# Performance work log

Hardware: AMD Instinct MI355X
Metric: run time of the kernel (lower is better)

Reference implementation:

```python
import jax, jax.numpy as jnp
import numpy as np

D_MODEL = 1024
N_HEAD = 16
N_KV_HEAD = 4
D_K = D_MODEL // N_HEAD          # 64
N_REP = N_HEAD // N_KV_HEAD      # 4
B, S = 2, 2048


def setup_inputs() -> dict:
    key = jax.random.key(0)
    ks = jax.random.split(key, 7)
    scale = 1.0 / np.sqrt(D_MODEL)
    return {
        "q": jax.random.normal(ks[0], (B, S, D_MODEL), jnp.float32),
        "k": jax.random.normal(ks[1], (B, S, D_MODEL), jnp.float32),
        "v": jax.random.normal(ks[2], (B, S, D_MODEL), jnp.float32),
        # weights stored [in, out] (nn.Linear applies x @ W.T; we fold the transpose)
        "W_q": jax.random.normal(ks[3], (D_MODEL, N_HEAD * D_K), jnp.float32) * scale,
        "W_k": jax.random.normal(ks[4], (D_MODEL, N_KV_HEAD * D_K), jnp.float32) * scale,
        "W_v": jax.random.normal(ks[5], (D_MODEL, N_KV_HEAD * D_K), jnp.float32) * scale,
        "W_o": jax.random.normal(ks[6], (D_MODEL, D_MODEL), jnp.float32) * scale,
    }


def reference(q, k, v, W_q, W_k, W_v, W_o):
    batch, seq_q, _ = q.shape
    seq_k = k.shape[1]
    # projections -> [b, h, s, d]
    Q = (q @ W_q).reshape(batch, seq_q, N_HEAD, D_K).transpose(0, 2, 1, 3)
    K = (k @ W_k).reshape(batch, seq_k, N_KV_HEAD, D_K).transpose(0, 2, 1, 3)
    V = (v @ W_v).reshape(batch, seq_k, N_KV_HEAD, D_K).transpose(0, 2, 1, 3)
    # repeat each KV head n_rep times consecutively (matches expand+reshape)
    K = jnp.repeat(K, N_REP, axis=1)  # [b, n_head, seq_k, d_k]
    V = jnp.repeat(V, N_REP, axis=1)
    scores = jnp.einsum('bhqd,bhkd->bhqk', Q, K) / np.sqrt(D_K).astype(jnp.float32)
    attn = jax.nn.softmax(scores, axis=-1)
    out = jnp.einsum('bhqk,bhkd->bhqd', attn, V)  # [b, h, seq_q, d_k]
    out = out.transpose(0, 2, 1, 3).reshape(batch, seq_q, D_MODEL)
    return out @ W_o
```

## Files before the change

kernel.cpp:

```cpp
#include <hip/hip_runtime.h>
#include <hip/hip_bf16.h>
#include <stdint.h>

#define DEVINL __device__ __forceinline__

typedef unsigned short u16;
typedef __bf16 bf16x8 __attribute__((ext_vector_type(8)));
typedef float f32x4 __attribute__((ext_vector_type(4)));
typedef float f32x16 __attribute__((ext_vector_type(16)));
typedef unsigned short u16x8 __attribute__((ext_vector_type(8)));
typedef unsigned int u32x4 __attribute__((ext_vector_type(4)));

constexpr int BATCH = 2, SEQ = 2048, DM = 1024, NH = 16, NKVH = 4, DK = 64;
#define QSCALE 0.18033688f

DEVINL u16 f2bf(float f) {
    unsigned u = __builtin_bit_cast(unsigned, f);
    u += 0x7fffu + ((u >> 16) & 1u);
    return (u16)(u >> 16);
}

DEVINL unsigned pkbf(float a, float b) {
    unsigned r;
    asm("v_cvt_pk_bf16_f32 %0, %1, %2" : "=v"(r) : "v"(a), "v"(b));
    return r;
}
DEVINL void swap32(unsigned& a, unsigned& b) {
    asm("v_permlane32_swap_b32 %0, %1" : "+v"(a), "+v"(b));
}
DEVINL float fexp2(float x) {
    float r;
    asm("v_exp_f32 %0, %1" : "=v"(r) : "v"(x));
    return r;
}

DEVINL void gload16(const void* g, void* l) {
    __builtin_amdgcn_global_load_lds(
        (const __attribute__((address_space(1))) unsigned int*)g,
        (__attribute__((address_space(3))) unsigned int*)l, 16, 0, 0);
}

DEVINL bf16x8 ldfrag(const u16* p) { return *reinterpret_cast<const bf16x8*>(p); }

__global__ __launch_bounds__(256) void prep_kernel(
    const float* __restrict__ Wq, const float* __restrict__ Wk,
    const float* __restrict__ Wv, const float* __restrict__ Wo,
    u16* __restrict__ Wqt, u16* __restrict__ Wkt,
    u16* __restrict__ Wvt, u16* __restrict__ Wot) {
    __shared__ float tile[32][33];
    int bid = blockIdx.x;
    int z = bid >> 10, rem = bid & 1023;
    const float* W;
    u16* Wt;
    int N;
    switch (z) {
        case 0: W = Wq; Wt = Wqt; N = 1024; break;
        case 1: W = Wk; Wt = Wkt; N = 256; break;
        case 2: W = Wv; Wt = Wvt; N = 256; break;
        default: W = Wo; Wt = Wot; N = 1024; break;
    }
    int n0 = (rem & 31) * 32;
    if (n0 >= N) return;
    int k0 = (rem >> 5) * 32;
    int tx = threadIdx.x & 31, ty = threadIdx.x >> 5;
#pragma unroll
    for (int r = 0; r < 4; ++r)
        tile[ty + 8 * r][tx] = W[(size_t)(k0 + ty + 8 * r) * N + n0 + tx];
    __syncthreads();
#pragma unroll
    for (int r = 0; r < 4; ++r)
        Wt[(size_t)(n0 + ty + 8 * r) * 1024 + k0 + tx] = f2bf(tile[tx][ty + 8 * r]);
}

#define GEMM_CORE64(Apt, Bpt)                                                 \
    __shared__ __align__(16) u16 Al[2][128 * 64];                             \
    __shared__ __align__(16) u16 Bl[2][64 * 64];                              \
    const int tid = threadIdx.x;                                              \
    const int lane = tid & 63;                                                \
    const int w = tid >> 6;                                                   \
    const u16* Ab = (Apt) + (size_t)m0 * 1024;                                \
    const u16* Bb = (Bpt) + (size_t)n0 * 1024;                                \
    f32x4 acc[2][4] = {};                                                     \
    auto stage = [&](int buf, int kt) {                                       \
        _Pragma("unroll") for (int rnd = 0; rnd < 4; ++rnd) {                 \
            int L = tid * 16 + rnd * 4096;                                    \
            int row = L >> 7;                                                 \
            int cb = (L & 127) ^ ((row & 7) << 4);                            \
            gload16(Ab + (size_t)row * 1024 + kt * 64 + (cb >> 1),            \
                    &Al[buf][L >> 1]);                                        \
        }                                                                     \
        _Pragma("unroll") for (int rnd = 0; rnd < 2; ++rnd) {                 \
            int L = tid * 16 + rnd * 4096;                                    \
            int row = L >> 7;                                                 \
            int cb = (L & 127) ^ ((row & 7) << 4);                            \
            gload16(Bb + (size_t)row * 1024 + kt * 64 + (cb >> 1),            \
                    &Bl[buf][L >> 1]);                                        \
        }                                                                     \
    };                                                                        \
    stage(0, 0);                                                              \
    __syncthreads();                                                          \
    int buf = 0;                                                              \
    for (int kt = 0; kt < 16; ++kt) {                                         \
        if (kt + 1 < 16) stage(buf ^ 1, kt + 1);                              \
        bf16x8 af[2][2], bfr[2][4];                                           \
        _Pragma("unroll") for (int kk = 0; kk < 2; ++kk)                      \
            _Pragma("unroll") for (int mi = 0; mi < 2; ++mi) {                \
                int row = w * 32 + mi * 16 + (lane & 15);                     \
                int cb = (kk * 64 + (lane >> 4) * 16) ^ ((row & 7) << 4);     \
                af[kk][mi] = ldfrag(&Al[buf][row * 64 + (cb >> 1)]);          \
            }                                                                 \
        _Pragma("unroll") for (int kk = 0; kk < 2; ++kk)                      \
            _Pragma("unroll") for (int ni = 0; ni < 4; ++ni) {                \
                int row = ni * 16 + (lane & 15);                              \
                int cb = (kk * 64 + (lane >> 4) * 16) ^ ((row & 7) << 4);     \
                bfr[kk][ni] = ldfrag(&Bl[buf][row * 64 + (cb >> 1)]);         \
            }                                                                 \
        _Pragma("unroll") for (int kk = 0; kk < 2; ++kk)                      \
            _Pragma("unroll") for (int mi = 0; mi < 2; ++mi)                  \
                _Pragma("unroll") for (int ni = 0; ni < 4; ++ni)              \
                    acc[mi][ni] = __builtin_amdgcn_mfma_f32_16x16x32_bf16(    \
                        af[kk][mi], bfr[kk][ni], acc[mi][ni], 0, 0, 0);       \
        __syncthreads();                                                      \
        buf ^= 1;                                                             \
    }

__global__ __launch_bounds__(256) void proj_kernel(
    const float* __restrict__ q32, const float* __restrict__ k32, const float* __restrict__ v32,
    const u16* __restrict__ Wqt, const u16* __restrict__ Wkt, const u16* __restrict__ Wvt,
    u16* __restrict__ Qp, u16* __restrict__ Kf, u16* __restrict__ Vf) {
    int bid = blockIdx.x;
    int tile = (bid & 7) * 96 + (bid >> 3);
    const float* A32;
    const u16* Bt;
    int m0, n0, z;
    if (tile < 512) {
        z = 0; A32 = q32; Bt = Wqt; m0 = (tile >> 4) * 128; n0 = (tile & 15) * 64;
    } else if (tile < 640) {
        int t = tile - 512;
        z = 1; A32 = k32; Bt = Wkt; m0 = (t >> 2) * 128; n0 = (t & 3) * 64;
    } else {
        int t = tile - 640;
        z = 2; A32 = v32; Bt = Wvt; m0 = (t >> 2) * 128; n0 = (t & 3) * 64;
    }

    __shared__ __align__(16) u16 Al[2][128 * 64];
    __shared__ __align__(16) u16 Bl[2][64 * 64];
    const int tid = threadIdx.x;
    const int lane = tid & 63;
    const int w = tid >> 6;
    const float* Ab32 = A32 + (size_t)m0 * 1024;
    const u16* Bb = Bt + (size_t)n0 * 1024;
    f32x4 acc[2][4] = {};

    int adst[4];
    const float* asrc[4];
#pragma unroll
    for (int rnd = 0; rnd < 4; ++rnd) {
        int L = tid * 16 + rnd * 4096;
        int row = L >> 7, colb = L & 127;
        adst[rnd] = (row * 128 + (colb ^ ((row & 7) << 4)));
        asrc[rnd] = Ab32 + (size_t)row * 1024 + (colb >> 1);
    }
    const int LB = tid * 16;
    const int brow0 = LB >> 7;
    const int bcb0 = (LB & 127) ^ ((brow0 & 7) << 4);
    const int LB1 = LB + 4096;
    const int brow1 = LB1 >> 7;
    const int bcb1 = (LB1 & 127) ^ ((brow1 & 7) << 4);

    auto stageB = [&](int buf, int kt) {
        gload16(Bb + (size_t)brow0 * 1024 + kt * 64 + (bcb0 >> 1), &Bl[buf][LB >> 1]);
        gload16(Bb + (size_t)brow1 * 1024 + kt * 64 + (bcb1 >> 1), &Bl[buf][LB1 >> 1]);
    };
    auto packwr = [&](int buf, const float4& a, const float4& b, int dst) {
        u32x4 pk;
        pk[0] = pkbf(a.x, a.y); pk[1] = pkbf(a.z, a.w);
        pk[2] = pkbf(b.x, b.y); pk[3] = pkbf(b.z, b.w);
        *(u32x4*)((char*)&Al[buf][0] + dst) = pk;
    };

    {
        stageB(0, 0);
#pragma unroll
        for (int rnd = 0; rnd < 4; ++rnd) {
            float4 a = *(const float4*)asrc[rnd];
            float4 b = *(const float4*)(asrc[rnd] + 4);
            packwr(0, a, b, adst[rnd]);
        }
    }
    __syncthreads();

    int buf = 0;
    for (int kt = 0; kt < 16; ++kt) {
        float4 a4[4], b4[4];
        if (kt + 1 < 16) {
            stageB(buf ^ 1, kt + 1);
#pragma unroll
            for (int rnd = 0; rnd < 4; ++rnd) {
                const float* s = asrc[rnd] + (kt + 1) * 64;
                a4[rnd] = *(const float4*)s;
                b4[rnd] = *(const float4*)(s + 4);
            }
        }
        bf16x8 af[2][2], bfr[2][4];
#pragma unroll
        for (int kk = 0; kk < 2; ++kk)
#pragma unroll
            for (int mi = 0; mi < 2; ++mi) {
                int row = w * 32 + mi * 16 + (lane & 15);
                int cb = (kk * 64 + (lane >> 4) * 16) ^ ((row & 7) << 4);
                af[kk][mi] = ldfrag(&Al[buf][row * 64 + (cb >> 1)]);
            }
#pragma unroll
        for (int kk = 0; kk < 2; ++kk)
#pragma unroll
            for (int ni = 0; ni < 4; ++ni) {
                int row = ni * 16 + (lane & 15);
                int cb = (kk * 64 + (lane >> 4) * 16) ^ ((row & 7) << 4);
                bfr[kk][ni] = ldfrag(&Bl[buf][row * 64 + (cb >> 1)]);
            }
#pragma unroll
        for (int kk = 0; kk < 2; ++kk)
#pragma unroll
            for (int mi = 0; mi < 2; ++mi)
#pragma unroll
                for (int ni = 0; ni < 4; ++ni)
                    acc[mi][ni] = __builtin_amdgcn_mfma_f32_16x16x32_bf16(
                        af[kk][mi], bfr[kk][ni], acc[mi][ni], 0, 0, 0);
        if (kt + 1 < 16) {
#pragma unroll
            for (int rnd = 0; rnd < 4; ++rnd)
                packwr(buf ^ 1, a4[rnd], b4[rnd], adst[rnd]);
        }
        __syncthreads();
        buf ^= 1;
    }

#pragma unroll
    for (int mi = 0; mi < 2; ++mi)
#pragma unroll
        for (int ni = 0; ni < 4; ++ni)
#pragma unroll
            for (int r = 0; r < 4; ++r) {
                int row = m0 + w * 32 + mi * 16 + (lane >> 4) * 4 + r;
                int col = n0 + ni * 16 + (lane & 15);
                float v = acc[mi][ni][r];
                int bb = row >> 11, s = row & 2047;
                int hh = col >> 6, dd = col & 63;
                if (z == 0) {
                    Qp[((((size_t)bb * NH + hh) * 2048 + s) << 6) + dd] = f2bf(v * QSCALE);
                } else if (z == 1) {
                    size_t base = (size_t)(bb * NKVH + hh) * 131072;
                    int s32 = s >> 5, q31s = s & 31;
                    int c = dd >> 4, hib = (dd >> 3) & 1, j = dd & 7;
                    Kf[base + (size_t)((s32 * 4 + c) * 64 + hib * 32 + q31s) * 8 + j] = f2bf(v);
                } else {
                    size_t base = (size_t)(bb * NKVH + hh) * 131072;
                    int kt = s >> 6, i = (s >> 4) & 3, hib = (s >> 3) & 1, j = s & 7;
                    int dt = dd >> 5, q31v = dd & 31;
                    Vf[base + (size_t)((((kt * 2 + dt) * 4 + i) * 64) + hib * 32 + q31v) * 8 + j] = f2bf(v);
                }
            }
}

__global__ __launch_bounds__(256) void oproj_kernel(const u16* __restrict__ Oa,
                                                    const u16* __restrict__ Wot,
                                                    float* __restrict__ out) {
    int bid = blockIdx.x;
    int tile = (bid & 7) * 64 + (bid >> 3);
    const int m0 = (tile >> 4) * 128, n0 = (tile & 15) * 64;

    GEMM_CORE64(Oa, Wot)

#pragma unroll
    for (int mi = 0; mi < 2; ++mi)
#pragma unroll
        for (int ni = 0; ni < 4; ++ni)
#pragma unroll
            for (int r = 0; r < 4; ++r) {
                int row = m0 + w * 32 + mi * 16 + (lane >> 4) * 4 + r;
                int col = n0 + ni * 16 + (lane & 15);
                out[(size_t)row * 1024 + col] = acc[mi][ni][r];
            }
}

__global__ __launch_bounds__(256) void attn_kernel(const u16* __restrict__ Qp,
                                                   const u16* __restrict__ Kf,
                                                   const u16* __restrict__ Vf,
                                                   u16* __restrict__ Oa) {
    const int tid = threadIdx.x;
    const int lane = tid & 63, w = tid >> 6;
    const int hi = lane >> 5, q31 = lane & 31;
    const int qt = blockIdx.x, h = blockIdx.y, b = blockIdx.z;
    const int kvh = h >> 2;
    const int qrow = qt * 128 + w * 32 + q31;

    const u16* Qb = Qp + ((size_t)((b * NH + h) * SEQ) + qrow) * 64 + hi * 8;
    bf16x8 qf0 = ldfrag(Qb), qf1 = ldfrag(Qb + 16);
    bf16x8 qf2 = ldfrag(Qb + 32), qf3 = ldfrag(Qb + 48);

    const u16* Kb = Kf + (size_t)(b * NKVH + kvh) * 131072 + lane * 8;
    const u16* Vb = Vf + (size_t)(b * NKVH + kvh) * 131072 + lane * 8;

    bf16x8 k0[8], k1[8], vf[8];
#pragma unroll
    for (int r = 0; r < 8; ++r) k0[r] = ldfrag(Kb + (size_t)r * 512);
#pragma unroll
    for (int r = 0; r < 8; ++r) k1[r] = ldfrag(Kb + (size_t)(8 + r) * 512);
#pragma unroll
    for (int r = 0; r < 8; ++r) vf[r] = ldfrag(Vb + (size_t)r * 512);

    u16x8 ov;
#pragma unroll
    for (int j = 0; j < 8; ++j) ov[j] = 0x3F80;
    const bf16x8 ones = __builtin_bit_cast(bf16x8, ov);

    f32x16 od0 = {}, od1 = {}, lacc = {};
    f32x16 sA0 = {}, sA1 = {}, sB0 = {}, sB1 = {};

    sA0 = __builtin_amdgcn_mfma_f32_32x32x16_bf16(k0[0], qf0, sA0, 0, 0, 0);
    sA1 = __builtin_amdgcn_mfma_f32_32x32x16_bf16(k0[4], qf0, sA1, 0, 0, 0);
    sA0 = __builtin_amdgcn_mfma_f32_32x32x16_bf16(k0[1], qf1, sA0, 0, 0, 0);
    sA1 = __builtin_amdgcn_mfma_f32_32x32x16_bf16(k0[5], qf1, sA1, 0, 0, 0);
    sA0 = __builtin_amdgcn_mfma_f32_32x32x16_bf16(k0[2], qf2, sA0, 0, 0, 0);
    sA1 = __builtin_amdgcn_mfma_f32_32x32x16_bf16(k0[6], qf2, sA1, 0, 0, 0);
    sA0 = __builtin_amdgcn_mfma_f32_32x32x16_bf16(k0[3], qf3, sA0, 0, 0, 0);
    sA1 = __builtin_amdgcn_mfma_f32_32x32x16_bf16(k0[7], qf3, sA1, 0, 0, 0);

#define PACKP(sv, s, outf)                                    \
        {                                                     \
            unsigned x0 = pkbf(sv[8 * s + 0], sv[8 * s + 1]); \
            unsigned x1 = pkbf(sv[8 * s + 2], sv[8 * s + 3]); \
            unsigned y0 = pkbf(sv[8 * s + 4], sv[8 * s + 5]); \
            unsigned y1 = pkbf(sv[8 * s + 6], sv[8 * s + 7]); \
            swap32(x0, y0);                                   \
            swap32(x1, y1);                                   \
            u32x4 tt2 = {x0, x1, y0, y1};                     \
            outf = __builtin_bit_cast(bf16x8, tt2);           \
        }

#define BODY(SC0, SC1, SN0, SN1, KQK, KLD, KIDX, VIDX)                        \
    {                                                                         \
        __builtin_amdgcn_s_setprio(1);                                        \
        SN0 = {};                                                             \
        SN1 = {};                                                             \
        SN0 = __builtin_amdgcn_mfma_f32_32x32x16_bf16(KQK[0], qf0, SN0, 0, 0, 0); \
        SN1 = __builtin_amdgcn_mfma_f32_32x32x16_bf16(KQK[4], qf0, SN1, 0, 0, 0); \
        SN0 = __builtin_amdgcn_mfma_f32_32x32x16_bf16(KQK[1], qf1, SN0, 0, 0, 0); \
        SN1 = __builtin_amdgcn_mfma_f32_32x32x16_bf16(KQK[5], qf1, SN1, 0, 0, 0); \
        SN0 = __builtin_amdgcn_mfma_f32_32x32x16_bf16(KQK[2], qf2, SN0, 0, 0, 0); \
        SN1 = __builtin_amdgcn_mfma_f32_32x32x16_bf16(KQK[6], qf2, SN1, 0, 0, 0); \
        SN0 = __builtin_amdgcn_mfma_f32_32x32x16_bf16(KQK[3], qf3, SN0, 0, 0, 0); \
        SN1 = __builtin_amdgcn_mfma_f32_32x32x16_bf16(KQK[7], qf3, SN1, 0, 0, 0); \
        __builtin_amdgcn_s_setprio(0);                                        \
        _Pragma("unroll") for (int r = 0; r < 8; ++r)                         \
            KLD[r] = ldfrag(Kb + (size_t)((KIDX) * 8 + r) * 512);             \
        _Pragma("unroll") for (int r = 0; r < 16; ++r) {                      \
            SC0[r] = fexp2(SC0[r]);                                           \
            SC1[r] = fexp2(SC1[r]);                                           \
        }                                                                     \
        bf16x8 pa0, pa1, pa2, pa3;                                            \
        PACKP(SC0, 0, pa0)                                                    \
        PACKP(SC0, 1, pa1)                                                    \
        PACKP(SC1, 0, pa2)                                                    \
        PACKP(SC1, 1, pa3)                                                    \
        __builtin_amdgcn_s_setprio(1);                                        \
        lacc = __builtin_amdgcn_mfma_f32_32x32x16_bf16(ones, pa0, lacc, 0, 0, 0); \
        od0 = __builtin_amdgcn_mfma_f32_32x32x16_bf16(vf[0], pa0, od0, 0, 0, 0); \
        od1 = __builtin_amdgcn_mfma_f32_32x32x16_bf16(vf[4], pa0, od1, 0, 0, 0); \
        lacc = __builtin_amdgcn_mfma_f32_32x32x16_bf16(ones, pa1, lacc, 0, 0, 0); \
        od0 = __builtin_amdgcn_mfma_f32_32x32x16_bf16(vf[1], pa1, od0, 0, 0, 0); \
        od1 = __builtin_amdgcn_mfma_f32_32x32x16_bf16(vf[5], pa1, od1, 0, 0, 0); \
        lacc = __builtin_amdgcn_mfma_f32_32x32x16_bf16(ones, pa2, lacc, 0, 0, 0); \
        od0 = __builtin_amdgcn_mfma_f32_32x32x16_bf16(vf[2], pa2, od0, 0, 0, 0); \
        od1 = __builtin_amdgcn_mfma_f32_32x32x16_bf16(vf[6], pa2, od1, 0, 0, 0); \
        lacc = __builtin_amdgcn_mfma_f32_32x32x16_bf16(ones, pa3, lacc, 0, 0, 0); \
        od0 = __builtin_amdgcn_mfma_f32_32x32x16_bf16(vf[3], pa3, od0, 0, 0, 0); \
        od1 = __builtin_amdgcn_mfma_f32_32x32x16_bf16(vf[7], pa3, od1, 0, 0, 0); \
        __builtin_amdgcn_s_setprio(0);                                        \
        _Pragma("unroll") for (int r = 0; r < 8; ++r)                         \
            vf[r] = ldfrag(Vb + (size_t)((VIDX) * 8 + r) * 512);              \
    }

    for (int tt = 0; tt < 16; ++tt) {
        int t = tt * 2;
        BODY(sA0, sA1, sB0, sB1, k1, k0, (t + 2) & 31, (t + 1) & 31)
        BODY(sB0, sB1, sA0, sA1, k0, k1, (t + 3) & 31, (t + 2) & 31)
    }
#undef BODY
#undef PACKP

    float inv = 1.0f / lacc[0];
    u16* Ob = Oa + ((size_t)(b * SEQ) + qrow) * DM + h * 64;
#pragma unroll
    for (int i = 0; i < 8; ++i) {
        int r = 2 * i;
        int d = (r & 3) + 8 * (r >> 2) + 4 * hi;
        *(unsigned*)(Ob + d) = pkbf(od0[r] * inv, od0[r + 1] * inv);
        *(unsigned*)(Ob + 32 + d) = pkbf(od1[r] * inv, od1[r + 1] * inv);
    }
}

extern "C" void kernel_launch(void* const* d_in, const int* in_sizes, int n_in,
                              void* d_out, int out_size, void* d_ws, size_t ws_size,
                              hipStream_t stream) {
    const float* q  = (const float*)d_in[0];
    const float* k  = (const float*)d_in[1];
    const float* v  = (const float*)d_in[2];
    const float* Wq = (const float*)d_in[3];
    const float* Wk = (const float*)d_in[4];
    const float* Wv = (const float*)d_in[5];
    const float* Wo = (const float*)d_in[6];
    float* out = (float*)d_out;

    char* ws = (char*)d_ws;
    u16* Wqt = (u16*)(ws + (size_t)0);
    u16* Wkt = (u16*)(ws + ((size_t)2 << 20));
    u16* Wvt = (u16*)(ws + ((size_t)3 << 20));
    u16* Wot = (u16*)(ws + ((size_t)4 << 20));
    u16* Qp  = (u16*)(ws + ((size_t)6 << 20));
    u16* Kf  = (u16*)(ws + ((size_t)14 << 20));
    u16* Vf  = (u16*)(ws + ((size_t)16 << 20));
    u16* Oa  = (u16*)(ws + ((size_t)18 << 20));

    prep_kernel<<<4096, 256, 0, stream>>>(Wq, Wk, Wv, Wo, Wqt, Wkt, Wvt, Wot);

    proj_kernel<<<768, 256, 0, stream>>>(q, k, v, Wqt, Wkt, Wvt, Qp, Kf, Vf);

    attn_kernel<<<dim3(16, 16, 2), 256, 0, stream>>>(Qp, Kf, Vf, Oa);

    oproj_kernel<<<512, 256, 0, stream>>>(Oa, Wot, out);
}
```

Baseline: 103.4 us.

## Process two 32-row query tiles per wave and compute softmax denominator with VALU

Each wave now handles 64 query rows as two 32-row tiles that share every loaded K and V fragment, which halves K/V global loads per query row. The key tile per step shrinks from 64 to 32. The MFMA against a ones vector that produced the row sum is replaced by VALU adds of the exponentials plus one cross-lane shuffle, removing a quarter of the PV-phase MFMAs. The grid is halved to 256 blocks, which lowers parallelism on the device and raises register pressure from the extra accumulators.

```diff
diff --git a/kernel.cpp b/kernel.cpp
--- a/kernel.cpp
+++ b/kernel.cpp
@@ -293,39 +293,40 @@
     const int hi = lane >> 5, q31 = lane & 31;
     const int qt = blockIdx.x, h = blockIdx.y, b = blockIdx.z;
     const int kvh = h >> 2;
-    const int qrow = qt * 128 + w * 32 + q31;
-
-    const u16* Qb = Qp + ((size_t)((b * NH + h) * SEQ) + qrow) * 64 + hi * 8;
-    bf16x8 qf0 = ldfrag(Qb), qf1 = ldfrag(Qb + 16);
-    bf16x8 qf2 = ldfrag(Qb + 32), qf3 = ldfrag(Qb + 48);
+    const int qb0 = qt * 256 + w * 64 + q31;
+
+    const u16* QbA = Qp + ((size_t)((b * NH + h) * SEQ) + qb0) * 64 + hi * 8;
+    const u16* QbB = QbA + (size_t)32 * 64;
+    bf16x8 qfA0 = ldfrag(QbA), qfA1 = ldfrag(QbA + 16);
+    bf16x8 qfA2 = ldfrag(QbA + 32), qfA3 = ldfrag(QbA + 48);
+    bf16x8 qfB0 = ldfrag(QbB), qfB1 = ldfrag(QbB + 16);
+    bf16x8 qfB2 = ldfrag(QbB + 32), qfB3 = ldfrag(QbB + 48);
 
     const u16* Kb = Kf + (size_t)(b * NKVH + kvh) * 131072 + lane * 8;
     const u16* Vb = Vf + (size_t)(b * NKVH + kvh) * 131072 + lane * 8;
 
-    bf16x8 k0[8], k1[8], vf[8];
-#pragma unroll
-    for (int r = 0; r < 8; ++r) k0[r] = ldfrag(Kb + (size_t)r * 512);
-#pragma unroll
-    for (int r = 0; r < 8; ++r) k1[r] = ldfrag(Kb + (size_t)(8 + r) * 512);
-#pragma unroll
-    for (int r = 0; r < 8; ++r) vf[r] = ldfrag(Vb + (size_t)r * 512);
-
-    u16x8 ov;
-#pragma unroll
-    for (int j = 0; j < 8; ++j) ov[j] = 0x3F80;
-    const bf16x8 ones = __builtin_bit_cast(bf16x8, ov);
-
-    f32x16 od0 = {}, od1 = {}, lacc = {};
-    f32x16 sA0 = {}, sA1 = {}, sB0 = {}, sB1 = {};
-
-    sA0 = __builtin_amdgcn_mfma_f32_32x32x16_bf16(k0[0], qf0, sA0, 0, 0, 0);
-    sA1 = __builtin_amdgcn_mfma_f32_32x32x16_bf16(k0[4], qf0, sA1, 0, 0, 0);
-    sA0 = __builtin_amdgcn_mfma_f32_32x32x16_bf16(k0[1], qf1, sA0, 0, 0, 0);
-    sA1 = __builtin_amdgcn_mfma_f32_32x32x16_bf16(k0[5], qf1, sA1, 0, 0, 0);
-    sA0 = __builtin_amdgcn_mfma_f32_32x32x16_bf16(k0[2], qf2, sA0, 0, 0, 0);
-    sA1 = __builtin_amdgcn_mfma_f32_32x32x16_bf16(k0[6], qf2, sA1, 0, 0, 0);
-    sA0 = __builtin_amdgcn_mfma_f32_32x32x16_bf16(k0[3], qf3, sA0, 0, 0, 0);
-    sA1 = __builtin_amdgcn_mfma_f32_32x32x16_bf16(k0[7], qf3, sA1, 0, 0, 0);
+    bf16x8 kA[4], kB[4], vf[4];
+#pragma unroll
+    for (int c = 0; c < 4; ++c) kA[c] = ldfrag(Kb + (size_t)c * 512);
+#pragma unroll
+    for (int c = 0; c < 4; ++c) kB[c] = ldfrag(Kb + (size_t)(4 + c) * 512);
+    vf[0] = ldfrag(Vb + (size_t)0 * 512);
+    vf[1] = ldfrag(Vb + (size_t)1 * 512);
+    vf[2] = ldfrag(Vb + (size_t)4 * 512);
+    vf[3] = ldfrag(Vb + (size_t)5 * 512);
+
+    f32x16 odA0 = {}, odA1 = {}, odB0 = {}, odB1 = {};
+    float lsumA = 0.f, lsumB = 0.f;
+    f32x16 sAA = {}, sAB = {}, sBA = {}, sBB = {};
+
+    sAA = __builtin_amdgcn_mfma_f32_32x32x16_bf16(kA[0], qfA0, sAA, 0, 0, 0);
+    sAB = __builtin_amdgcn_mfma_f32_32x32x16_bf16(kA[0], qfB0, sAB, 0, 0, 0);
+    sAA = __builtin_amdgcn_mfma_f32_32x32x16_bf16(kA[1], qfA1, sAA, 0, 0, 0);
+    sAB = __builtin_amdgcn_mfma_f32_32x32x16_bf16(kA[1], qfB1, sAB, 0, 0, 0);
+    sAA = __builtin_amdgcn_mfma_f32_32x32x16_bf16(kA[2], qfA2, sAA, 0, 0, 0);
+    sAB = __builtin_amdgcn_mfma_f32_32x32x16_bf16(kA[2], qfB2, sAB, 0, 0, 0);
+    sAA = __builtin_amdgcn_mfma_f32_32x32x16_bf16(kA[3], qfA3, sAA, 0, 0, 0);
+    sAB = __builtin_amdgcn_mfma_f32_32x32x16_bf16(kA[3], qfB3, sAB, 0, 0, 0);
 
 #define PACKP(sv, s, outf)                                    \
         {                                                     \
@@ -339,65 +340,89 @@
             outf = __builtin_bit_cast(bf16x8, tt2);           \
         }
 
-#define BODY(SC0, SC1, SN0, SN1, KQK, KLD, KIDX, VIDX)                        \
+#define BODY(SCA, SCB, SNA, SNB, KQK, KLD, T)                                 \
     {                                                                         \
         __builtin_amdgcn_s_setprio(1);                                        \
-        SN0 = {};                                                             \
-        SN1 = {};                                                             \
-        SN0 = __builtin_amdgcn_mfma_f32_32x32x16_bf16(KQK[0], qf0, SN0, 0, 0, 0); \
-        SN1 = __builtin_amdgcn_mfma_f32_32x32x16_bf16(KQK[4], qf0, SN1, 0, 0, 0); \
-        SN0 = __builtin_amdgcn_mfma_f32_32x32x16_bf16(KQK[1], qf1, SN0, 0, 0, 0); \
-        SN1 = __builtin_amdgcn_mfma_f32_32x32x16_bf16(KQK[5], qf1, SN1, 0, 0, 0); \
-        SN0 = __builtin_amdgcn_mfma_f32_32x32x16_bf16(KQK[2], qf2, SN0, 0, 0, 0); \
-        SN1 = __builtin_amdgcn_mfma_f32_32x32x16_bf16(KQK[6], qf2, SN1, 0, 0, 0); \
-        SN0 = __builtin_amdgcn_mfma_f32_32x32x16_bf16(KQK[3], qf3, SN0, 0, 0, 0); \
-        SN1 = __builtin_amdgcn_mfma_f32_32x32x16_bf16(KQK[7], qf3, SN1, 0, 0, 0); \
+        SNA = {};                                                             \
+        SNB = {};                                                             \
+        SNA = __builtin_amdgcn_mfma_f32_32x32x16_bf16(KQK[0], qfA0, SNA, 0, 0, 0); \
+        SNB = __builtin_amdgcn_mfma_f32_32x32x16_bf16(KQK[0], qfB0, SNB, 0, 0, 0); \
+        SNA = __builtin_amdgcn_mfma_f32_32x32x16_bf16(KQK[1], qfA1, SNA, 0, 0, 0); \
+        SNB = __builtin_amdgcn_mfma_f32_32x32x16_bf16(KQK[1], qfB1, SNB, 0, 0, 0); \
+        SNA = __builtin_amdgcn_mfma_f32_32x32x16_bf16(KQK[2], qfA2, SNA, 0, 0, 0); \
+        SNB = __builtin_amdgcn_mfma_f32_32x32x16_bf16(KQK[2], qfB2, SNB, 0, 0, 0); \
+        SNA = __builtin_amdgcn_mfma_f32_32x32x16_bf16(KQK[3], qfA3, SNA, 0, 0, 0); \
+        SNB = __builtin_amdgcn_mfma_f32_32x32x16_bf16(KQK[3], qfB3, SNB, 0, 0, 0); \
         __builtin_amdgcn_s_setprio(0);                                        \
-        _Pragma("unroll") for (int r = 0; r < 8; ++r)                         \
-            KLD[r] = ldfrag(Kb + (size_t)((KIDX) * 8 + r) * 512);             \
+        {                                                                     \
+            int kc = (((T) + 2) & 63) * 4;                                    \
+            _Pragma("unroll") for (int c = 0; c < 4; ++c)                     \
+                KLD[c] = ldfrag(Kb + (size_t)(kc + c) * 512);                 \
+        }                                                                     \
         _Pragma("unroll") for (int r = 0; r < 16; ++r) {                      \
-            SC0[r] = fexp2(SC0[r]);                                           \
-            SC1[r] = fexp2(SC1[r]);                                           \
-        }                                                                     \
-        bf16x8 pa0, pa1, pa2, pa3;                                            \
-        PACKP(SC0, 0, pa0)                                                    \
-        PACKP(SC0, 1, pa1)                                                    \
-        PACKP(SC1, 0, pa2)                                                    \
-        PACKP(SC1, 1, pa3)                                                    \
+            SCA[r] = fexp2(SCA[r]);                                           \
+            SCB[r] = fexp2(SCB[r]);                                           \
+        }                                                                     \
+        {                                                                     \
+            float uA0 = (SCA[0] + SCA[1]) + (SCA[2] + SCA[3]);                \
+            float uA1 = (SCA[4] + SCA[5]) + (SCA[6] + SCA[7]);                \
+            float uA2 = (SCA[8] + SCA[9]) + (SCA[10] + SCA[11]);              \
+            float uA3 = (SCA[12] + SCA[13]) + (SCA[14] + SCA[15]);            \
+            lsumA += (uA0 + uA1) + (uA2 + uA3);                               \
+            float uB0 = (SCB[0] + SCB[1]) + (SCB[2] + SCB[3]);                \
+            float uB1 = (SCB[4] + SCB[5]) + (SCB[6] + SCB[7]);                \
+            float uB2 = (SCB[8] + SCB[9]) + (SCB[10] + SCB[11]);              \
+            float uB3 = (SCB[12] + SCB[13]) + (SCB[14] + SCB[15]);            \
+            lsumB += (uB0 + uB1) + (uB2 + uB3);                               \
+        }                                                                     \
+        bf16x8 paA0, paA1, paB0, paB1;                                        \
+        PACKP(SCA, 0, paA0)                                                   \
+        PACKP(SCA, 1, paA1)                                                   \
+        PACKP(SCB, 0, paB0)                                                   \
+        PACKP(SCB, 1, paB1)                                                   \
         __builtin_amdgcn_s_setprio(1);                                        \
-        lacc = __builtin_amdgcn_mfma_f32_32x32x16_bf16(ones, pa0, lacc, 0, 0, 0); \
-        od0 = __builtin_amdgcn_mfma_f32_32x32x16_bf16(vf[0], pa0, od0, 0, 0, 0); \
-        od1 = __builtin_amdgcn_mfma_f32_32x32x16_bf16(vf[4], pa0, od1, 0, 0, 0); \
-        lacc = __builtin_amdgcn_mfma_f32_32x32x16_bf16(ones, pa1, lacc, 0, 0, 0); \
-        od0 = __builtin_amdgcn_mfma_f32_32x32x16_bf16(vf[1], pa1, od0, 0, 0, 0); \
-        od1 = __builtin_amdgcn_mfma_f32_32x32x16_bf16(vf[5], pa1, od1, 0, 0, 0); \
-        lacc = __builtin_amdgcn_mfma_f32_32x32x16_bf16(ones, pa2, lacc, 0, 0, 0); \
-        od0 = __builtin_amdgcn_mfma_f32_32x32x16_bf16(vf[2], pa2, od0, 0, 0, 0); \
-        od1 = __builtin_amdgcn_mfma_f32_32x32x16_bf16(vf[6], pa2, od1, 0, 0, 0); \
-        lacc = __builtin_amdgcn_mfma_f32_32x32x16_bf16(ones, pa3, lacc, 0, 0, 0); \
-        od0 = __builtin_amdgcn_mfma_f32_32x32x16_bf16(vf[3], pa3, od0, 0, 0, 0); \
-        od1 = __builtin_amdgcn_mfma_f32_32x32x16_bf16(vf[7], pa3, od1, 0, 0, 0); \
+        odA0 = __builtin_amdgcn_mfma_f32_32x32x16_bf16(vf[0], paA0, odA0, 0, 0, 0); \
+        odB0 = __builtin_amdgcn_mfma_f32_32x32x16_bf16(vf[0], paB0, odB0, 0, 0, 0); \
+        odA1 = __builtin_amdgcn_mfma_f32_32x32x16_bf16(vf[2], paA0, odA1, 0, 0, 0); \
+        odB1 = __builtin_amdgcn_mfma_f32_32x32x16_bf16(vf[2], paB0, odB1, 0, 0, 0); \
+        odA0 = __builtin_amdgcn_mfma_f32_32x32x16_bf16(vf[1], paA1, odA0, 0, 0, 0); \
+        odB0 = __builtin_amdgcn_mfma_f32_32x32x16_bf16(vf[1], paB1, odB0, 0, 0, 0); \
+        odA1 = __builtin_amdgcn_mfma_f32_32x32x16_bf16(vf[3], paA1, odA1, 0, 0, 0); \
+        odB1 = __builtin_amdgcn_mfma_f32_32x32x16_bf16(vf[3], paB1, odB1, 0, 0, 0); \
         __builtin_amdgcn_s_setprio(0);                                        \
-        _Pragma("unroll") for (int r = 0; r < 8; ++r)                         \
-            vf[r] = ldfrag(Vb + (size_t)((VIDX) * 8 + r) * 512);              \
-    }
-
-    for (int tt = 0; tt < 16; ++tt) {
+        {                                                                     \
+            int vi = ((T) + 1) & 63;                                          \
+            int vbase = (vi >> 1) * 8 + (vi & 1) * 2;                         \
+            vf[0] = ldfrag(Vb + (size_t)(vbase + 0) * 512);                   \
+            vf[1] = ldfrag(Vb + (size_t)(vbase + 1) * 512);                   \
+            vf[2] = ldfrag(Vb + (size_t)(vbase + 4) * 512);                   \
+            vf[3] = ldfrag(Vb + (size_t)(vbase + 5) * 512);                   \
+        }                                                                     \
+    }
+
+    for (int tt = 0; tt < 32; ++tt) {
         int t = tt * 2;
-        BODY(sA0, sA1, sB0, sB1, k1, k0, (t + 2) & 31, (t + 1) & 31)
-        BODY(sB0, sB1, sA0, sA1, k0, k1, (t + 3) & 31, (t + 2) & 31)
+        BODY(sAA, sAB, sBA, sBB, kB, kA, t)
+        BODY(sBA, sBB, sAA, sAB, kA, kB, t + 1)
     }
 #undef BODY
 #undef PACKP
 
-    float inv = 1.0f / lacc[0];
-    u16* Ob = Oa + ((size_t)(b * SEQ) + qrow) * DM + h * 64;
+    lsumA += __shfl_xor(lsumA, 32);
+    lsumB += __shfl_xor(lsumB, 32);
+
+    float invA = 1.0f / lsumA;
+    float invB = 1.0f / lsumB;
+    u16* ObA = Oa + ((size_t)(b * SEQ) + qb0) * DM + h * 64;
+    u16* ObB = ObA + (size_t)32 * DM;
 #pragma unroll
     for (int i = 0; i < 8; ++i) {
         int r = 2 * i;
         int d = (r & 3) + 8 * (r >> 2) + 4 * hi;
-        *(unsigned*)(Ob + d) = pkbf(od0[r] * inv, od0[r + 1] * inv);
-        *(unsigned*)(Ob + 32 + d) = pkbf(od1[r] * inv, od1[r + 1] * inv);
+        *(unsigned*)(ObA + d) = pkbf(odA0[r] * invA, odA0[r + 1] * invA);
+        *(unsigned*)(ObA + 32 + d) = pkbf(odA1[r] * invA, odA1[r + 1] * invA);
+        *(unsigned*)(ObB + d) = pkbf(odB0[r] * invB, odB0[r + 1] * invB);
+        *(unsigned*)(ObB + 32 + d) = pkbf(odB1[r] * invB, odB1[r + 1] * invB);
     }
 }
 
@@ -427,7 +452,7 @@
 
     proj_kernel<<<768, 256, 0, stream>>>(q, k, v, Wqt, Wkt, Wvt, Qp, Kf, Vf);
 
-    attn_kernel<<<dim3(16, 16, 2), 256, 0, stream>>>(Qp, Kf, Vf, Oa);
+    attn_kernel<<<dim3(8, 16, 2), 256, 0, stream>>>(Qp, Kf, Vf, Oa);
 
     oproj_kernel<<<512, 256, 0, stream>>>(Oa, Wot, out);
 }
```

Result: faster. 99.99 us (-3.3%).
